# Optimization experiments

Measured on AMD Instinct MI355X. Metric: run time of the kernel, lower is better.

Reference implementation:

```python
import jax, jax.numpy as jnp
import numpy as np
from jax import lax

B, C, L = 64, 12, 2048
KERN = 9
K = 8            # kernels per group
G = 64           # total groups -> divisor 2, _g = 32
_G = G // 2
N_PER = 6        # clip(C//2, 2, 8)
NUM_DIL = int(np.log2((L - 1) / (KERN - 1))) + 1  # 8


def _normalize(W):
    W = W - W.mean(-1, keepdims=True)
    return W / jnp.abs(W).sum(-1, keepdims=True)


def setup_inputs() -> dict:
    key = jax.random.key(0)
    kx, kw, ki = jax.random.split(key, 3)
    X = jax.random.normal(kx, (B, C, L), dtype=jnp.float32)
    W = _normalize(jax.random.normal(kw, (NUM_DIL, 2, K * _G, 1, KERN), dtype=jnp.float32))
    I = jax.random.randint(ki, (NUM_DIL, 2, _G, N_PER), 0, C, dtype=jnp.int32)
    return {"X": X, "W": W, "I": I}


def _branch(src, w, idx, d, p, k, g):
    # src: [B, C, L'], w: [k*g, 1, 9], idx: [g, n_per]
    b = src.shape[0]
    sel = src[:, idx].sum(2)  # [B, g, L'] channel-subset sum
    conv = lax.conv_general_dilated(
        sel, w, window_strides=(1,), padding=[(p, p)], rhs_dilation=(d,),
        dimension_numbers=("NCH", "OIH", "NCH"), feature_group_count=g,
    )  # [B, k*g, L']
    Zc = conv.reshape(b, g, k, -1)
    max_vals = Zc.max(2)            # [B, g, L']
    max_idx = Zc.argmax(2)          # [B, g, L'] in [0, k)
    min_idx = Zc.argmin(2)
    b_ix = jnp.arange(b)[:, None, None]
    g_ix = jnp.arange(g)[None, :, None]
    count_max = jnp.zeros((b, g, k), Zc.dtype).at[b_ix, g_ix, max_idx].add(max_vals)
    count_min = jnp.zeros((b, g, k), Zc.dtype).at[b_ix, g_ix, min_idx].add(1.0)
    return count_max, count_min


def reference(X, W, I):
    b = X.shape[0]
    k = W.shape[2] // I.shape[2]
    g = I.shape[2]
    num_dil = W.shape[0]
    diff_X = jnp.diff(X, axis=-1)
    outs = []
    for di in range(num_dil):
        d = 2 ** di
        p = ((KERN - 1) * d) // 2
        for diff in range(2):
            src = X if diff == 0 else diff_X
            cmax, cmin = _branch(src, W[di, diff], I[di, diff], d, p, k, g)
            outs.append(cmax)
            outs.append(cmin)
    Z = jnp.concatenate(outs, axis=1)  # [B, num_dil*2*2*g, k]
    return Z.reshape(b, -1)
```

## Files before the change

kernel.cpp:

```cpp
#include <hip/hip_runtime.h>
#include <stdint.h>

#define BB     64
#define CC     12
#define LL     2048
#define KERNSZ 9
#define KK     8
#define GG     32
#define NPER   6
#define NDIL   8
#define PAD    256
#define MAIN   2048
#define BUFSZ  (PAD + MAIN + PAD)
#define WPB    4

typedef float f2 __attribute__((ext_vector_type(2)));
typedef float f4 __attribute__((ext_vector_type(4)));

__device__ __forceinline__ void pk_fma_bcast(f2& acc, const f2& t, uint64_t wpair) {
    asm("v_pk_fma_f32 %0, %1, %2, %0 op_sel:[0,0,0] op_sel_hi:[0,1,1]"
        : "+v"(acc) : "v"(t), "s"(wpair));
}
__device__ __forceinline__ f2 pk_mul_bcast(const f2& t, uint64_t wpair) {
    f2 d;
    asm("v_pk_mul_f32 %0, %1, %2 op_sel:[0,0] op_sel_hi:[0,1]"
        : "=v"(d) : "v"(t), "s"(wpair));
    return d;
}
__device__ __forceinline__ float max3f(float a, float b, float c) {
    float d; asm("v_max3_f32 %0, %1, %2, %3" : "=v"(d) : "v"(a), "v"(b), "v"(c)); return d;
}
__device__ __forceinline__ float min3f(float a, float b, float c) {
    float d; asm("v_min3_f32 %0, %1, %2, %3" : "=v"(d) : "v"(a), "v"(b), "v"(c)); return d;
}

template <int D>
__device__ __forceinline__ void run_phase2(
    const float* __restrict__ sel, int lane, int dif,
    const uint64_t (&wp)[4][KERNSZ], float (&accM)[KK], uint32_t (&cnt)[KK])
{
    const float NANF = __uint_as_float(0x7fc00000u);

    #pragma unroll 2
    for (int q = 0; q < 32; ++q) {
        const int pos = q * 64 + lane;

        f2 t[KERNSZ];
        if constexpr (D == 128) {
            #pragma unroll
            for (int j = 0; j < KERNSZ; ++j) {
                int off = pos + (j - 4) * D;
                if (j < 4) off = (off < -PAD) ? -PAD : off;
                if (j > 4) off = (off > MAIN + PAD - 1) ? (MAIN + PAD - 1) : off;
                t[j].x = sel[off];
            }
        } else {
            const float* p = sel + pos - 4 * D;
            #pragma unroll
            for (int j = 0; j < KERNSZ; ++j)
                t[j].x = p[j * D];
        }

        f2 v2[4];
        #pragma unroll
        for (int c = 0; c < 4; ++c)
            v2[c] = pk_mul_bcast(t[0], wp[c][0]);
        #pragma unroll
        for (int j = 1; j < KERNSZ; ++j)
            #pragma unroll
            for (int c = 0; c < 4; ++c)
                pk_fma_bcast(v2[c], t[j], wp[c][j]);

        float v[KK] = { v2[0].x, v2[0].y, v2[1].x, v2[1].y,
                        v2[2].x, v2[2].y, v2[3].x, v2[3].y };

        float ma = max3f(v[0], v[1], v[2]);
        float mb = max3f(v[3], v[4], v[5]);
        float mc = max3f(v[6], v[7], ma);
        float mv = fmaxf(mb, mc);
        float na = min3f(v[0], v[1], v[2]);
        float nb = min3f(v[3], v[4], v[5]);
        float nc = min3f(v[6], v[7], na);
        float nv = fminf(nb, nc);

        if (dif && q == 31) {
            if (lane == 63) { mv = NANF; nv = NANF; }
        }

        #pragma unroll
        for (int k = 0; k < KK; ++k) {
            accM[k] += (v[k] == mv) ? v[k] : 0.0f;
            cnt[k] += (uint32_t)__popcll(__ballot(v[k] == nv));
        }
    }
}

__global__ __launch_bounds__(256, 4) void hydra_kernel(
    const float* __restrict__ X,
    const float* __restrict__ W,
    const int*   __restrict__ I,
    float*       __restrict__ out)
{
    __shared__ float lds[WPB][BUFSZ];

    const int tid  = threadIdx.x;
    const int wave = tid >> 6;
    const int lane = tid & 63;
    const int wid  = blockIdx.x * WPB + wave;
    const int b   = wid >> 9;
    const int r   = wid & 511;
    const int di  = r >> 6;
    const int r2  = r & 63;
    const int dif = r2 >> 5;
    const int g   = r2 & 31;

    float* buf = lds[wave];
    float* sel = buf + PAD;

    {
        f4 z = {0.0f, 0.0f, 0.0f, 0.0f};
        ((f4*)buf)[lane]                = z;
        ((f4*)(buf + PAD + MAIN))[lane] = z;
    }

    const int* Ig = I + ((size_t)((di * 2 + dif) * GG + g)) * NPER;
    const float* xb = X + (size_t)b * CC * LL;
    const f4* c0 = (const f4*)(xb + Ig[0] * LL);
    const f4* c1 = (const f4*)(xb + Ig[1] * LL);
    const f4* c2 = (const f4*)(xb + Ig[2] * LL);
    const f4* c3 = (const f4*)(xb + Ig[3] * LL);
    const f4* c4 = (const f4*)(xb + Ig[4] * LL);
    const f4* c5 = (const f4*)(xb + Ig[5] * LL);
    f4* sel4 = (f4*)sel;

    #pragma unroll 2
    for (int q = 0; q < 8; ++q) {
        int idx = q * 64 + lane;
        f4 s = (c0[idx] + c1[idx]) + (c2[idx] + c3[idx]) + (c4[idx] + c5[idx]);
        sel4[idx] = s;
    }

    if (dif) {
        #pragma unroll 2
        for (int q = 0; q < 8; ++q) {
            int idx = q * 64 + lane;
            f4 a  = sel4[idx];
            float an = sel[idx * 4 + 4];
            f4 v;
            v.x = a.y - a.x;
            v.y = a.z - a.y;
            v.z = a.w - a.z;
            v.w = (idx == 511) ? 0.0f : (an - a.w);
            sel4[idx] = v;
        }
    }

    const float* Wg = W + (size_t)((di * 2 + dif) * (KK * GG) + g * KK) * KERNSZ;
    uint64_t wp[4][KERNSZ];
    #pragma unroll
    for (int c = 0; c < 4; ++c)
        #pragma unroll
        for (int j = 0; j < KERNSZ; ++j) {
            uint32_t lo = __float_as_uint(Wg[(2 * c)     * KERNSZ + j]);
            uint32_t hi = __float_as_uint(Wg[(2 * c + 1) * KERNSZ + j]);
            wp[c][j] = (uint64_t)lo | ((uint64_t)hi << 32);
        }

    float    accM[KK];
    uint32_t cnt[KK];
    #pragma unroll
    for (int k = 0; k < KK; ++k) { accM[k] = 0.0f; cnt[k] = 0u; }

    switch (di) {
        case 0: run_phase2<1>  (sel, lane, dif, wp, accM, cnt); break;
        case 1: run_phase2<2>  (sel, lane, dif, wp, accM, cnt); break;
        case 2: run_phase2<4>  (sel, lane, dif, wp, accM, cnt); break;
        case 3: run_phase2<8>  (sel, lane, dif, wp, accM, cnt); break;
        case 4: run_phase2<16> (sel, lane, dif, wp, accM, cnt); break;
        case 5: run_phase2<32> (sel, lane, dif, wp, accM, cnt); break;
        case 6: run_phase2<64> (sel, lane, dif, wp, accM, cnt); break;
        default: run_phase2<128>(sel, lane, dif, wp, accM, cnt); break;
    }

    float* o = out + (size_t)b * 8192 + (size_t)((di * 2 + dif) * 2) * 256 + g * KK;
    #pragma unroll
    for (int k = 0; k < KK; ++k) {
        float a = accM[k];
        #pragma unroll
        for (int off = 32; off > 0; off >>= 1)
            a += __shfl_xor(a, off, 64);
        if (lane == 0) {
            o[k]       = a;
            o[256 + k] = (float)cnt[k];
        }
    }
}

extern "C" void kernel_launch(void* const* d_in, const int* in_sizes, int n_in,
                              void* d_out, int out_size, void* d_ws, size_t ws_size,
                              hipStream_t stream) {
    const float* X = (const float*)d_in[0];
    const float* W = (const float*)d_in[1];
    const int*   I = (const int*)d_in[2];
    float* out = (float*)d_out;

    const int total_waves = BB * NDIL * 2 * GG;
    const int blocks = total_waves / WPB;
    hydra_kernel<<<blocks, 256, 0, stream>>>(X, W, I, out);
}
```

Before: 252.1 us.

## Use one-wave blocks and software-pipeline LDS tap loads with double buffering

Each block now holds a single 64-thread wave with its own LDS buffer instead of four waves per block, so waves schedule independently. The inner convolution loop is restructured to double-buffer the tap loads: the next position's LDS reads are issued before computing the current one. The goal is to hide LDS latency and scheduling granularity, at the cost of more registers for two tap sets and more small blocks to launch.

```diff
diff --git a/kernel.cpp b/kernel.cpp
--- a/kernel.cpp
+++ b/kernel.cpp
@@ -12,7 +12,6 @@
 #define PAD    256
 #define MAIN   2048
 #define BUFSZ  (PAD + MAIN + PAD)
-#define WPB    4
 
 typedef float f2 __attribute__((ext_vector_type(2)));
 typedef float f4 __attribute__((ext_vector_type(4)));
@@ -35,78 +34,88 @@
 }
 
 template <int D>
+__device__ __forceinline__ void load_taps(const float* __restrict__ sel,
+                                          int pos, f2 (&t)[KERNSZ]) {
+    if constexpr (D == 128) {
+        #pragma unroll
+        for (int j = 0; j < KERNSZ; ++j) {
+            int off = pos + (j - 4) * D;
+            if (j < 4) off = (off < -PAD) ? -PAD : off;
+            if (j > 4) off = (off > MAIN + PAD - 1) ? (MAIN + PAD - 1) : off;
+            t[j].x = sel[off];
+        }
+    } else {
+        const float* p = sel + pos - 4 * D;
+        #pragma unroll
+        for (int j = 0; j < KERNSZ; ++j)
+            t[j].x = p[j * D];
+    }
+}
+
+__device__ __forceinline__ void conv_body(
+    const f2 (&t)[KERNSZ], const uint64_t (&wp)[4][KERNSZ],
+    bool kill63, int lane, float (&accM)[KK], uint32_t (&cnt)[KK])
+{
+    f2 v2[4];
+    #pragma unroll
+    for (int c = 0; c < 4; ++c)
+        v2[c] = pk_mul_bcast(t[0], wp[c][0]);
+    #pragma unroll
+    for (int j = 1; j < KERNSZ; ++j)
+        #pragma unroll
+        for (int c = 0; c < 4; ++c)
+            pk_fma_bcast(v2[c], t[j], wp[c][j]);
+
+    float v[KK] = { v2[0].x, v2[0].y, v2[1].x, v2[1].y,
+                    v2[2].x, v2[2].y, v2[3].x, v2[3].y };
+
+    float ma = max3f(v[0], v[1], v[2]);
+    float mb = max3f(v[3], v[4], v[5]);
+    float mc = max3f(v[6], v[7], ma);
+    float mv = fmaxf(mb, mc);
+    float na = min3f(v[0], v[1], v[2]);
+    float nb = min3f(v[3], v[4], v[5]);
+    float nc = min3f(v[6], v[7], na);
+    float nv = fminf(nb, nc);
+
+    if (kill63 && lane == 63) {
+        const float NANF = __uint_as_float(0x7fc00000u);
+        mv = NANF; nv = NANF;
+    }
+
+    #pragma unroll
+    for (int k = 0; k < KK; ++k) {
+        accM[k] += (v[k] == mv) ? v[k] : 0.0f;
+        cnt[k] += (uint32_t)__popcll(__ballot(v[k] == nv));
+    }
+}
+
+template <int D>
 __device__ __forceinline__ void run_phase2(
     const float* __restrict__ sel, int lane, int dif,
     const uint64_t (&wp)[4][KERNSZ], float (&accM)[KK], uint32_t (&cnt)[KK])
 {
-    const float NANF = __uint_as_float(0x7fc00000u);
-
-    #pragma unroll 2
-    for (int q = 0; q < 32; ++q) {
-        const int pos = q * 64 + lane;
-
-        f2 t[KERNSZ];
-        if constexpr (D == 128) {
-            #pragma unroll
-            for (int j = 0; j < KERNSZ; ++j) {
-                int off = pos + (j - 4) * D;
-                if (j < 4) off = (off < -PAD) ? -PAD : off;
-                if (j > 4) off = (off > MAIN + PAD - 1) ? (MAIN + PAD - 1) : off;
-                t[j].x = sel[off];
-            }
-        } else {
-            const float* p = sel + pos - 4 * D;
-            #pragma unroll
-            for (int j = 0; j < KERNSZ; ++j)
-                t[j].x = p[j * D];
-        }
-
-        f2 v2[4];
-        #pragma unroll
-        for (int c = 0; c < 4; ++c)
-            v2[c] = pk_mul_bcast(t[0], wp[c][0]);
-        #pragma unroll
-        for (int j = 1; j < KERNSZ; ++j)
-            #pragma unroll
-            for (int c = 0; c < 4; ++c)
-                pk_fma_bcast(v2[c], t[j], wp[c][j]);
-
-        float v[KK] = { v2[0].x, v2[0].y, v2[1].x, v2[1].y,
-                        v2[2].x, v2[2].y, v2[3].x, v2[3].y };
-
-        float ma = max3f(v[0], v[1], v[2]);
-        float mb = max3f(v[3], v[4], v[5]);
-        float mc = max3f(v[6], v[7], ma);
-        float mv = fmaxf(mb, mc);
-        float na = min3f(v[0], v[1], v[2]);
-        float nb = min3f(v[3], v[4], v[5]);
-        float nc = min3f(v[6], v[7], na);
-        float nv = fminf(nb, nc);
-
-        if (dif && q == 31) {
-            if (lane == 63) { mv = NANF; nv = NANF; }
-        }
-
-        #pragma unroll
-        for (int k = 0; k < KK; ++k) {
-            accM[k] += (v[k] == mv) ? v[k] : 0.0f;
-            cnt[k] += (uint32_t)__popcll(__ballot(v[k] == nv));
-        }
-    }
-}
-
-__global__ __launch_bounds__(256, 4) void hydra_kernel(
+    f2 tA[KERNSZ], tB[KERNSZ];
+    load_taps<D>(sel, lane, tA);
+    for (int q = 0; q < 32; q += 2) {
+        load_taps<D>(sel, (q + 1) * 64 + lane, tB);
+        conv_body(tA, wp, false, lane, accM, cnt);
+        if (q + 2 < 32)
+            load_taps<D>(sel, (q + 2) * 64 + lane, tA);
+        conv_body(tB, wp, dif && (q == 30), lane, accM, cnt);
+    }
+}
+
+__global__ __launch_bounds__(64, 4) void hydra_kernel(
     const float* __restrict__ X,
     const float* __restrict__ W,
     const int*   __restrict__ I,
     float*       __restrict__ out)
 {
-    __shared__ float lds[WPB][BUFSZ];
-
-    const int tid  = threadIdx.x;
-    const int wave = tid >> 6;
-    const int lane = tid & 63;
-    const int wid  = blockIdx.x * WPB + wave;
+    __shared__ float buf[BUFSZ];
+
+    const int lane = threadIdx.x;
+    const int wid  = blockIdx.x;
     const int b   = wid >> 9;
     const int r   = wid & 511;
     const int di  = r >> 6;
@@ -114,7 +123,6 @@
     const int dif = r2 >> 5;
     const int g   = r2 & 31;
 
-    float* buf = lds[wave];
     float* sel = buf + PAD;
 
     {
@@ -205,6 +213,5 @@
     float* out = (float*)d_out;
 
     const int total_waves = BB * NDIL * 2 * GG;
-    const int blocks = total_waves / WPB;
-    hydra_kernel<<<blocks, 256, 0, stream>>>(X, W, I, out);
-}
+    hydra_kernel<<<total_waves, 64, 0, stream>>>(X, W, I, out);
+}
```

New measurement: 243.5 us. 3.4% less time.
